# Kernel tuning notes

Measured on AMD Instinct MI355X. Metric: run time of the kernel, lower is better.

## Reference

```python
import jax, jax.numpy as jnp
import numpy as np

N_LAYERS = 5
D = 300        # pretrained GIN hidden dim
D_HID = 600
BN_EPS = 1e-5
IN_DIM = 256
HID = 128
OUT_DIM = 1


def setup_inputs() -> dict:
    key = jax.random.key(0)
    ks = jax.random.split(key, 24)
    N, E, G = 200_000, 800_000, 8192
    s = 0.02
    return {
        # graph structure / categorical features
        "atomic_number": jax.random.randint(ks[0], (N,), 0, 120),
        "chirality_type": jax.random.randint(ks[1], (N,), 0, 3),
        "bond_type": jax.random.randint(ks[2], (E,), 0, 6),
        "bond_direction_type": jax.random.randint(ks[3], (E,), 0, 3),
        "src": jax.random.randint(ks[4], (E,), 0, N),
        "dst": jax.random.randint(ks[5], (E,), 0, N),
        "graph_id": jnp.sort(jax.random.randint(ks[6], (N,), 0, G)),
        "n_graphs": G,
        # pretrained GIN params
        "emb_atom": jax.random.normal(ks[7], (120, D)) * s,
        "emb_chir": jax.random.normal(ks[8], (3, D)) * s,
        "edge_bond": jax.random.normal(ks[9], (N_LAYERS, 6, D)) * s,
        "edge_dir": jax.random.normal(ks[10], (N_LAYERS, 3, D)) * s,
        "W1": jax.random.normal(ks[11], (N_LAYERS, D, D_HID)) * s,
        "b1": jnp.zeros((N_LAYERS, D_HID)),
        "W2": jax.random.normal(ks[12], (N_LAYERS, D_HID, D)) * s,
        "b2": jnp.zeros((N_LAYERS, D)),
        "bn_gamma": jnp.ones((N_LAYERS, D)),
        "bn_beta": jnp.zeros((N_LAYERS, D)),
        "bn_mean": jax.random.normal(ks[13], (N_LAYERS, D)) * s,
        "bn_var": jax.random.uniform(ks[14], (N_LAYERS, D), minval=0.5, maxval=1.5),
        # head params
        "Wt": jax.random.normal(ks[15], (D, IN_DIM)) * s,
        "bt": jnp.zeros((IN_DIM,)),
        "Wh": jax.random.normal(ks[16], (IN_DIM, HID)) * s,
        "bh": jnp.zeros((HID,)),
        "Wf": jax.random.normal(ks[17], (HID, OUT_DIM)) * s,
        "bf": jnp.zeros((OUT_DIM,)),
    }


def reference(atomic_number, chirality_type, bond_type, bond_direction_type,
              src, dst, graph_id, n_graphs,
              emb_atom, emb_chir, edge_bond, edge_dir,
              W1, b1, W2, b2, bn_gamma, bn_beta, bn_mean, bn_var,
              Wt, bt, Wh, bh, Wf, bf):
    N = atomic_number.shape[0]
    # input node embedding (sum of categorical embeddings)
    h = emb_atom[atomic_number] + emb_chir[chirality_type]  # [N, D]

    for l in range(N_LAYERS):
        e = edge_bond[l][bond_type] + edge_dir[l][bond_direction_type]  # [E, D]
        msg = h[src] + e                                                # gather
        agg = jax.ops.segment_sum(msg, dst, num_segments=N)             # scatter-add
        z = h + agg                                                     # GIN eps=0 self term
        z = jax.nn.relu(z @ W1[l] + b1[l]) @ W2[l] + b2[l]              # MLP 300->600->300
        # BatchNorm in eval mode (running stats)
        z = (z - bn_mean[l]) * (bn_gamma[l] / jnp.sqrt(bn_var[l] + BN_EPS)) + bn_beta[l]
        h = jax.nn.relu(z) if l < N_LAYERS - 1 else z

    # AvgPooling readout: segment mean per graph
    sums = jax.ops.segment_sum(h, graph_id, num_segments=n_graphs)      # [G, D]
    cnts = jax.ops.segment_sum(jnp.ones((N,), h.dtype), graph_id, num_segments=n_graphs)
    x = sums / jnp.maximum(cnts, 1.0)[:, None]

    x = x @ Wt + bt                      # transform: Linear(300, in_dim)
    x = jax.nn.leaky_relu(x @ Wh + bh)   # hidden layer + LeakyReLU
    # dropout is identity in eval mode
    return x @ Wf + bf                   # [G, out_dim]
```

## Files before the change

### kernel.cpp

```cpp
#include <hip/hip_runtime.h>
#include <hip/hip_bf16.h>

#define D_NODE 300
#define DHID   600
#define NLAYER 5
#define NG     8192
#define BN_EPS 1e-5f
#define KP1    320
#define KP2    608
#define PER1   (DHID * KP1)
#define PER2   (D_NODE * KP2)

typedef unsigned short u16;
typedef unsigned int   u32;
typedef unsigned long long u64;
using f32x4   = __attribute__((ext_vector_type(4))) float;
using short8  = __attribute__((ext_vector_type(8))) short;
using short4v = __attribute__((ext_vector_type(4))) short;

__device__ __forceinline__ float bf2f(u16 u) {
    union { unsigned int i; float f; } v; v.i = ((unsigned int)u) << 16; return v.f;
}
__device__ __forceinline__ u16 f2bf(float f) {
    union { float f; unsigned int i; } v; v.f = f;
    unsigned int x = v.i;
    return (u16)((x + 0x7FFFu + ((x >> 16) & 1u)) >> 16);
}

__global__ __launch_bounds__(256) void embed_kernel(
    const int* __restrict__ an, const int* __restrict__ ct,
    const float* __restrict__ emb_atom, const float* __restrict__ emb_chir,
    u16* __restrict__ h, long total)
{
    long idx = (long)blockIdx.x * blockDim.x + threadIdx.x;
    if (idx >= total) return;
    int n = (int)(idx / 75);
    int c = (int)(idx % 75);
    int a = an[n], cc = ct[n];
    const float4 av = *(const float4*)&emb_atom[(long)a * D_NODE + c * 4];
    const float4 cv = *(const float4*)&emb_chir[(long)cc * D_NODE + c * 4];
    ushort4 o;
    o.x = f2bf(av.x + cv.x);
    o.y = f2bf(av.y + cv.y);
    o.z = f2bf(av.z + cv.z);
    o.w = f2bf(av.w + cv.w);
    *(ushort4*)&h[(long)n * D_NODE + c * 4] = o;
}

__global__ __launch_bounds__(256) void wconv_split(
    const float* __restrict__ W, u16* __restrict__ WbT,
    int K, int N, int KP, long per, long total)
{
    long idx = (long)blockIdx.x * blockDim.x + threadIdx.x;
    if (idx >= total) return;
    int l = (int)(idx / per);
    long r = idx % per;
    int n = (int)(r / KP);
    int k = (int)(r % KP);
    float v = (k < K) ? W[(long)l * K * N + (long)k * N + n] : 0.f;
    u16 hi = f2bf(v);
    float lo = v - bf2f(hi);
    WbT[(long)(2 * l) * per + r]     = hi;
    WbT[(long)(2 * l + 1) * per + r] = f2bf(lo);
}

__global__ __launch_bounds__(256) void comb_kernel(
    const float* __restrict__ ebond, const float* __restrict__ edir,
    float* __restrict__ comb, long total)
{
    long idx = (long)blockIdx.x * blockDim.x + threadIdx.x;
    if (idx >= total) return;
    int l  = (int)(idx / (18 * 75));
    int r  = (int)(idx % (18 * 75));
    int cm = r / 75;
    int c4 = r % 75;
    const float4 eb = *(const float4*)&ebond[((long)l * 6 + cm / 3) * D_NODE + c4 * 4];
    const float4 ed = *(const float4*)&edir [((long)l * 3 + cm % 3) * D_NODE + c4 * 4];
    float4 o;
    o.x = eb.x + ed.x; o.y = eb.y + ed.y; o.z = eb.z + ed.z; o.w = eb.w + ed.w;
    *(float4*)&comb[((long)l * 18 + cm) * D_NODE + c4 * 4] = o;
}

__global__ __launch_bounds__(256) void zero_int_kernel(int* __restrict__ p, int n)
{
    int i = blockIdx.x * blockDim.x + threadIdx.x;
    if (i < n) p[i] = 0;
}
__global__ __launch_bounds__(256) void count_kernel(
    const int* __restrict__ dst, int* __restrict__ cnt, int E)
{
    int e = blockIdx.x * blockDim.x + threadIdx.x;
    if (e < E) atomicAdd(&cnt[dst[e]], 1);
}
__global__ __launch_bounds__(256) void scan1_kernel(
    const int* __restrict__ cnt, int* __restrict__ bsum, int N)
{
    __shared__ int red[256];
    int b = blockIdx.x, t = threadIdx.x;
    int i0 = b * 1024 + t * 4;
    int s = 0;
    #pragma unroll
    for (int j = 0; j < 4; ++j) { int i = i0 + j; if (i < N) s += cnt[i]; }
    red[t] = s; __syncthreads();
    for (int off = 128; off > 0; off >>= 1) {
        if (t < off) red[t] += red[t + off];
        __syncthreads();
    }
    if (t == 0) bsum[b] = red[0];
}
__global__ void scan2_kernel(int* __restrict__ bsum, int nb)
{
    if (threadIdx.x == 0 && blockIdx.x == 0) {
        int run = 0;
        for (int b = 0; b < nb; ++b) { int v = bsum[b]; bsum[b] = run; run += v; }
    }
}
__global__ __launch_bounds__(256) void scan3_kernel(
    const int* __restrict__ bsum, int* __restrict__ cnt,
    int* __restrict__ row_ptr, int N, int E)
{
    __shared__ int sbuf[256];
    int b = blockIdx.x, t = threadIdx.x;
    int i0 = b * 1024 + t * 4;
    int v[4]; int s = 0;
    #pragma unroll
    for (int j = 0; j < 4; ++j) { int i = i0 + j; v[j] = (i < N) ? cnt[i] : 0; s += v[j]; }
    sbuf[t] = s; __syncthreads();
    for (int off = 1; off < 256; off <<= 1) {
        int add = (t >= off) ? sbuf[t - off] : 0;
        __syncthreads();
        sbuf[t] += add;
        __syncthreads();
    }
    int base = bsum[b] + sbuf[t] - s;
    #pragma unroll
    for (int j = 0; j < 4; ++j) {
        int i = i0 + j;
        if (i < N) { row_ptr[i] = base; cnt[i] = base; base += v[j]; }
    }
    if (b == 0 && t == 0) row_ptr[N] = E;
}
__global__ __launch_bounds__(256) void fill_kernel(
    const int* __restrict__ src, const int* __restrict__ bt, const int* __restrict__ bd,
    const int* __restrict__ dst, int* __restrict__ fillp,
    u32* __restrict__ epack, int E)
{
    int e = blockIdx.x * blockDim.x + threadIdx.x;
    if (e < E) {
        int pos = atomicAdd(&fillp[dst[e]], 1);
        epack[pos] = (u32)src[e] | ((u32)(bt[e] * 3 + bd[e]) << 20);
    }
}

__global__ __launch_bounds__(256) void agg_kernel(
    const u16* __restrict__ h,
    const int* __restrict__ row_ptr, const u32* __restrict__ epack,
    const float* __restrict__ comb,
    u16* __restrict__ z, long total)
{
    long idx = (long)blockIdx.x * blockDim.x + threadIdx.x;
    if (idx >= total) return;
    int n = (int)(idx / 75);
    int c = (int)(idx % 75);
    const ushort4 hq = *(const ushort4*)&h[(long)n * D_NODE + c * 4];
    float a0 = bf2f(hq.x), a1 = bf2f(hq.y), a2 = bf2f(hq.z), a3 = bf2f(hq.w);
    int s0 = row_ptr[n], s1 = row_ptr[n + 1];
    for (int i = s0; i < s1; ++i) {
        u32 ep = epack[i];
        int s  = (int)(ep & 0xFFFFFu);
        int cm = (int)(ep >> 20);
        const ushort4 hv = *(const ushort4*)&h[(long)s * D_NODE + c * 4];
        const float4 cv = *(const float4*)&comb[(long)cm * D_NODE + c * 4];
        a0 += bf2f(hv.x) + cv.x;
        a1 += bf2f(hv.y) + cv.y;
        a2 += bf2f(hv.z) + cv.z;
        a3 += bf2f(hv.w) + cv.w;
    }
    ushort4 o;
    o.x = f2bf(a0); o.y = f2bf(a1); o.z = f2bf(a2); o.w = f2bf(a3);
    *(ushort4*)&z[(long)n * D_NODE + c * 4] = o;
}

__global__ __launch_bounds__(512, 1) void mlp_fused(
    const u16* __restrict__ Z,
    const u16* __restrict__ W1T,
    const u16* __restrict__ W2T,
    const float* __restrict__ b1, const float* __restrict__ b2,
    const float* __restrict__ bn_g, const float* __restrict__ bn_b,
    const float* __restrict__ bn_m, const float* __restrict__ bn_v,
    u16* __restrict__ Hout, int Nrows, int relu_out)
{
    __shared__ u16 As[128][328];
    __shared__ u16 Tc[128][136];
    const int tid  = threadIdx.x;
    const int lane = tid & 63;
    const int w    = tid >> 6;
    const int lrow = lane & 15;
    const int kg   = lane >> 4;
    const long r0  = (long)blockIdx.x * 128;
    const short8 zz = (short8){0,0,0,0,0,0,0,0};

    for (int i = tid; i < 128 * 80; i += 512) {
        int r = i / 80, c4 = i % 80;
        short4v v = (short4v){0, 0, 0, 0};
        if (c4 < 75 && r0 + r < Nrows)
            v = *(const short4v*)&Z[(r0 + r) * D_NODE + c4 * 4];
        *(short4v*)&As[r][c4 * 4] = v;
    }
    __syncthreads();

    f32x4 hacc[8][3];
    #pragma unroll
    for (int m = 0; m < 8; ++m)
        #pragma unroll
        for (int n = 0; n < 3; ++n)
            hacc[m][n] = (f32x4){0.f, 0.f, 0.f, 0.f};
    const u16* w2p[3]; bool w2v[3];
    #pragma unroll
    for (int nf = 0; nf < 3; ++nf) {
        int gn = w * 48 + nf * 16 + lrow;
        w2v[nf] = (gn < D_NODE);
        w2p[nf] = W2T + (long)gn * KP2 + kg * 8;
    }
    const bool p2_active = (w * 48 < D_NODE);

    for (int tc = 0; tc < 5; ++tc) {
        const int gn1 = tc * 128 + w * 16 + lrow;
        const bool v1 = (gn1 < DHID);
        const u16* w1p = W1T + (long)gn1 * KP1 + kg * 8;

        f32x4 p1[8];
        #pragma unroll
        for (int m = 0; m < 8; ++m) p1[m] = (f32x4){0.f, 0.f, 0.f, 0.f};

        short8 cwh = v1 ? *(const short8*)(w1p) : zz;

        #pragma unroll
        for (int k0i = 0; k0i < 10; ++k0i) {
            short8 nwh;
            if (k0i < 9) {
                nwh = v1 ? *(const short8*)(w1p + (k0i + 1) * 32) : zz;
            }
            {
                short8 a0 = *(const short8*)&As[ 0 + lrow][k0i * 32 + kg * 8];
                short8 a1 = *(const short8*)&As[16 + lrow][k0i * 32 + kg * 8];
                short8 a2 = *(const short8*)&As[32 + lrow][k0i * 32 + kg * 8];
                short8 a3 = *(const short8*)&As[48 + lrow][k0i * 32 + kg * 8];
                __builtin_amdgcn_s_setprio(1);
                p1[0] = __builtin_amdgcn_mfma_f32_16x16x32_bf16(a0, cwh, p1[0], 0, 0, 0);
                p1[1] = __builtin_amdgcn_mfma_f32_16x16x32_bf16(a1, cwh, p1[1], 0, 0, 0);
                p1[2] = __builtin_amdgcn_mfma_f32_16x16x32_bf16(a2, cwh, p1[2], 0, 0, 0);
                p1[3] = __builtin_amdgcn_mfma_f32_16x16x32_bf16(a3, cwh, p1[3], 0, 0, 0);
                __builtin_amdgcn_s_setprio(0);
            }
            {
                short8 a4 = *(const short8*)&As[ 64 + lrow][k0i * 32 + kg * 8];
                short8 a5 = *(const short8*)&As[ 80 + lrow][k0i * 32 + kg * 8];
                short8 a6 = *(const short8*)&As[ 96 + lrow][k0i * 32 + kg * 8];
                short8 a7 = *(const short8*)&As[112 + lrow][k0i * 32 + kg * 8];
                __builtin_amdgcn_s_setprio(1);
                p1[4] = __builtin_amdgcn_mfma_f32_16x16x32_bf16(a4, cwh, p1[4], 0, 0, 0);
                p1[5] = __builtin_amdgcn_mfma_f32_16x16x32_bf16(a5, cwh, p1[5], 0, 0, 0);
                p1[6] = __builtin_amdgcn_mfma_f32_16x16x32_bf16(a6, cwh, p1[6], 0, 0, 0);
                p1[7] = __builtin_amdgcn_mfma_f32_16x16x32_bf16(a7, cwh, p1[7], 0, 0, 0);
                __builtin_amdgcn_s_setprio(0);
            }
            if (k0i < 9) { cwh = nwh; }
        }

        {
            float bias = v1 ? b1[gn1] : 0.f;
            #pragma unroll
            for (int m = 0; m < 8; ++m)
                #pragma unroll
                for (int j = 0; j < 4; ++j) {
                    float v = fmaxf(p1[m][j] + bias, 0.f);
                    Tc[m * 16 + kg * 4 + j][w * 16 + lrow] = f2bf(v);
                }
        }
        __syncthreads();

        if (p2_active) {
            const int kbase = tc * 128;
            #pragma unroll
            for (int ks = 0; ks < 4; ++ks) {
                if (kbase + ks * 32 < KP2) {
                    const int kk = kbase + ks * 32;
                    short8 w2h0 = w2v[0] ? *(const short8*)(w2p[0] + kk) : zz;
                    short8 w2h1 = w2v[1] ? *(const short8*)(w2p[1] + kk) : zz;
                    short8 w2h2 = w2v[2] ? *(const short8*)(w2p[2] + kk) : zz;
                    {
                        short8 t0 = *(const short8*)&Tc[ 0 + lrow][ks * 32 + kg * 8];
                        short8 t1 = *(const short8*)&Tc[16 + lrow][ks * 32 + kg * 8];
                        short8 t2 = *(const short8*)&Tc[32 + lrow][ks * 32 + kg * 8];
                        short8 t3 = *(const short8*)&Tc[48 + lrow][ks * 32 + kg * 8];
                        __builtin_amdgcn_s_setprio(1);
                        hacc[0][0] = __builtin_amdgcn_mfma_f32_16x16x32_bf16(t0, w2h0, hacc[0][0], 0, 0, 0);
                        hacc[1][0] = __builtin_amdgcn_mfma_f32_16x16x32_bf16(t1, w2h0, hacc[1][0], 0, 0, 0);
                        hacc[2][0] = __builtin_amdgcn_mfma_f32_16x16x32_bf16(t2, w2h0, hacc[2][0], 0, 0, 0);
                        hacc[3][0] = __builtin_amdgcn_mfma_f32_16x16x32_bf16(t3, w2h0, hacc[3][0], 0, 0, 0);
                        hacc[0][1] = __builtin_amdgcn_mfma_f32_16x16x32_bf16(t0, w2h1, hacc[0][1], 0, 0, 0);
                        hacc[1][1] = __builtin_amdgcn_mfma_f32_16x16x32_bf16(t1, w2h1, hacc[1][1], 0, 0, 0);
                        hacc[2][1] = __builtin_amdgcn_mfma_f32_16x16x32_bf16(t2, w2h1, hacc[2][1], 0, 0, 0);
                        hacc[3][1] = __builtin_amdgcn_mfma_f32_16x16x32_bf16(t3, w2h1, hacc[3][1], 0, 0, 0);
                        hacc[0][2] = __builtin_amdgcn_mfma_f32_16x16x32_bf16(t0, w2h2, hacc[0][2], 0, 0, 0);
                        hacc[1][2] = __builtin_amdgcn_mfma_f32_16x16x32_bf16(t1, w2h2, hacc[1][2], 0, 0, 0);
                        hacc[2][2] = __builtin_amdgcn_mfma_f32_16x16x32_bf16(t2, w2h2, hacc[2][2], 0, 0, 0);
                        hacc[3][2] = __builtin_amdgcn_mfma_f32_16x16x32_bf16(t3, w2h2, hacc[3][2], 0, 0, 0);
                        __builtin_amdgcn_s_setprio(0);
                    }
                    {
                        short8 t4 = *(const short8*)&Tc[ 64 + lrow][ks * 32 + kg * 8];
                        short8 t5 = *(const short8*)&Tc[ 80 + lrow][ks * 32 + kg * 8];
                        short8 t6 = *(const short8*)&Tc[ 96 + lrow][ks * 32 + kg * 8];
                        short8 t7 = *(const short8*)&Tc[112 + lrow][ks * 32 + kg * 8];
                        __builtin_amdgcn_s_setprio(1);
                        hacc[4][0] = __builtin_amdgcn_mfma_f32_16x16x32_bf16(t4, w2h0, hacc[4][0], 0, 0, 0);
                        hacc[5][0] = __builtin_amdgcn_mfma_f32_16x16x32_bf16(t5, w2h0, hacc[5][0], 0, 0, 0);
                        hacc[6][0] = __builtin_amdgcn_mfma_f32_16x16x32_bf16(t6, w2h0, hacc[6][0], 0, 0, 0);
                        hacc[7][0] = __builtin_amdgcn_mfma_f32_16x16x32_bf16(t7, w2h0, hacc[7][0], 0, 0, 0);
                        hacc[4][1] = __builtin_amdgcn_mfma_f32_16x16x32_bf16(t4, w2h1, hacc[4][1], 0, 0, 0);
                        hacc[5][1] = __builtin_amdgcn_mfma_f32_16x16x32_bf16(t5, w2h1, hacc[5][1], 0, 0, 0);
                        hacc[6][1] = __builtin_amdgcn_mfma_f32_16x16x32_bf16(t6, w2h1, hacc[6][1], 0, 0, 0);
                        hacc[7][1] = __builtin_amdgcn_mfma_f32_16x16x32_bf16(t7, w2h1, hacc[7][1], 0, 0, 0);
                        hacc[4][2] = __builtin_amdgcn_mfma_f32_16x16x32_bf16(t4, w2h2, hacc[4][2], 0, 0, 0);
                        hacc[5][2] = __builtin_amdgcn_mfma_f32_16x16x32_bf16(t5, w2h2, hacc[5][2], 0, 0, 0);
                        hacc[6][2] = __builtin_amdgcn_mfma_f32_16x16x32_bf16(t6, w2h2, hacc[6][2], 0, 0, 0);
                        hacc[7][2] = __builtin_amdgcn_mfma_f32_16x16x32_bf16(t7, w2h2, hacc[7][2], 0, 0, 0);
                        __builtin_amdgcn_s_setprio(0);
                    }
                }
            }
        }
        __syncthreads();
    }

    #pragma unroll
    for (int nf = 0; nf < 3; ++nf) {
        int gn = w * 48 + nf * 16 + lrow;
        if (gn < D_NODE) {
            float bias = b2[gn];
            float sc = bn_g[gn] * rsqrtf(bn_v[gn] + BN_EPS);
            float mn = bn_m[gn], bb = bn_b[gn];
            #pragma unroll
            for (int m = 0; m < 8; ++m)
                #pragma unroll
                for (int j = 0; j < 4; ++j) {
                    long gr = r0 + m * 16 + kg * 4 + j;
                    if (gr < Nrows) {
                        float v = hacc[m][nf][j] + bias;
                        v = (v - mn) * sc + bb;
                        if (relu_out) v = fmaxf(v, 0.f);
                        Hout[gr * D_NODE + gn] = f2bf(v);
                    }
                }
        }
    }
}

__device__ __forceinline__ int lower_bound(const int* __restrict__ a, int n, int key)
{
    int lo = 0, hi = n;
    while (lo < hi) { int mid = (lo + hi) >> 1; if (a[mid] < key) lo = mid + 1; else hi = mid; }
    return lo;
}

__global__ __launch_bounds__(256) void pool_head1(
    const u16* __restrict__ h, const int* __restrict__ gid, int N,
    const float* __restrict__ Wt, const float* __restrict__ bt,
    float* __restrict__ x1)
{
    __shared__ float xs[304];
    __shared__ int se[2];
    int g = blockIdx.x;
    int t = threadIdx.x;
    if (t == 0) se[0] = lower_bound(gid, N, g);
    if (t == 1) se[1] = lower_bound(gid, N, g + 1);
    __syncthreads();
    int start = se[0], end = se[1];
    float inv = (end > start) ? 1.0f / (float)(end - start) : 0.f;
    float a0 = 0.f, a1 = 0.f;
    for (int n = start; n < end; ++n) {
        const u16* hp = &h[(long)n * D_NODE];
        a0 += bf2f(hp[t]);
        if (t < 44) a1 += bf2f(hp[256 + t]);
    }
    xs[t] = a0 * inv;
    if (t < 44) xs[256 + t] = a1 * inv;
    __syncthreads();
    float acc = bt[t];
    for (int k = 0; k < D_NODE; ++k)
        acc = fmaf(xs[k], Wt[(long)k * 256 + t], acc);
    x1[(long)g * 256 + t] = acc;
}

__global__ __launch_bounds__(128) void head2_kernel(
    const float* __restrict__ x1,
    const float* __restrict__ Wh, const float* __restrict__ bh,
    const float* __restrict__ Wf, const float* __restrict__ bf,
    float* __restrict__ out, int G)
{
    __shared__ float xs[256];
    __shared__ float red[128];
    int g = blockIdx.x;
    int t = threadIdx.x;
    for (int i = t; i < 256; i += 128) xs[i] = x1[(long)g * 256 + i];
    __syncthreads();
    float acc = bh[t];
    for (int k = 0; k < 256; ++k)
        acc = fmaf(xs[k], Wh[(long)k * 128 + t], acc);
    acc = acc > 0.f ? acc : 0.01f * acc;
    red[t] = acc * Wf[t];
    __syncthreads();
    for (int s = 64; s > 0; s >>= 1) {
        if (t < s) red[t] += red[t + s];
        __syncthreads();
    }
    if (t == 0) out[g] = red[0] + bf[0];
}

extern "C" void kernel_launch(void* const* d_in, const int* in_sizes, int n_in,
                              void* d_out, int out_size, void* d_ws, size_t ws_size,
                              hipStream_t stream)
{
    const int* an   = (const int*)d_in[0];
    const int* ct   = (const int*)d_in[1];
    const int* bt   = (const int*)d_in[2];
    const int* bd   = (const int*)d_in[3];
    const int* src  = (const int*)d_in[4];
    const int* dst  = (const int*)d_in[5];
    const int* gid  = (const int*)d_in[6];
    const float* emb_atom  = (const float*)d_in[8];
    const float* emb_chir  = (const float*)d_in[9];
    const float* edge_bond = (const float*)d_in[10];
    const float* edge_dir  = (const float*)d_in[11];
    const float* W1   = (const float*)d_in[12];
    const float* b1   = (const float*)d_in[13];
    const float* W2   = (const float*)d_in[14];
    const float* b2   = (const float*)d_in[15];
    const float* bn_g = (const float*)d_in[16];
    const float* bn_b = (const float*)d_in[17];
    const float* bn_m = (const float*)d_in[18];
    const float* bn_v = (const float*)d_in[19];
    const float* Wt   = (const float*)d_in[20];
    const float* btr  = (const float*)d_in[21];
    const float* Wh   = (const float*)d_in[22];
    const float* bh   = (const float*)d_in[23];
    const float* Wf   = (const float*)d_in[24];
    const float* bf   = (const float*)d_in[25];

    const long N = in_sizes[0];
    const long E = in_sizes[4];
    const int  G = NG;

    char* base = (char*)d_ws;
    size_t off = 0;
    u16* h  = (u16*)(base + off);           off += (size_t)N * D_NODE * 2;
    u16* z  = (u16*)(base + off);           off += (size_t)N * D_NODE * 2;
    u16* WbT1 = (u16*)(base + off);         off += (size_t)NLAYER * 2 * PER1 * 2;
    u16* WbT2 = (u16*)(base + off);         off += (size_t)NLAYER * 2 * PER2 * 2;
    float* comb = (float*)(base + off);     off += (size_t)NLAYER * 18 * D_NODE * 4;
    int* row_ptr = (int*)(base + off);      off += (((size_t)(N + 1) * 4) + 63) & ~(size_t)63;
    u32* epack = (u32*)(base + off);
    int* row_fill = (int*)z;
    int* bsum     = row_fill + N;
    float* x1     = (float*)z;

    const long nodeTot = N * 75;
    const int  blk = 256;
    const long nodeBlocks = (nodeTot + blk - 1) / blk;
    const int  SB = (int)((N + 1023) / 1024);

    {
        long t1 = (long)NLAYER * PER1;
        wconv_split<<<(t1 + blk - 1) / blk, blk, 0, stream>>>(
            W1, WbT1, D_NODE, DHID, KP1, (long)PER1, t1);
        long t2 = (long)NLAYER * PER2;
        wconv_split<<<(t2 + blk - 1) / blk, blk, 0, stream>>>(
            W2, WbT2, DHID, D_NODE, KP2, (long)PER2, t2);
    }
    {
        long tc = (long)NLAYER * 18 * 75;
        comb_kernel<<<(tc + blk - 1) / blk, blk, 0, stream>>>(
            edge_bond, edge_dir, comb, tc);
    }

    zero_int_kernel<<<((int)N + blk - 1) / blk, blk, 0, stream>>>(row_fill, (int)N);
    count_kernel<<<((int)E + blk - 1) / blk, blk, 0, stream>>>(dst, row_fill, (int)E);
    scan1_kernel<<<SB, blk, 0, stream>>>(row_fill, bsum, (int)N);
    scan2_kernel<<<1, 64, 0, stream>>>(bsum, SB);
    scan3_kernel<<<SB, blk, 0, stream>>>(bsum, row_fill, row_ptr, (int)N, (int)E);
    fill_kernel<<<((int)E + blk - 1) / blk, blk, 0, stream>>>(
        src, bt, bd, dst, row_fill, epack, (int)E);

    embed_kernel<<<nodeBlocks, blk, 0, stream>>>(an, ct, emb_atom, emb_chir, h, nodeTot);

    const int mlpBlocks = (int)((N + 127) / 128);
    for (int l = 0; l < NLAYER; ++l) {
        agg_kernel<<<nodeBlocks, blk, 0, stream>>>(
            h, row_ptr, epack,
            comb + (long)l * 18 * D_NODE,
            z, nodeTot);

        mlp_fused<<<mlpBlocks, 512, 0, stream>>>(
            z,
            WbT1 + (long)(2 * l) * PER1,
            WbT2 + (long)(2 * l) * PER2,
            b1 + (long)l * DHID, b2 + (long)l * D_NODE,
            bn_g + (long)l * D_NODE, bn_b + (long)l * D_NODE,
            bn_m + (long)l * D_NODE, bn_v + (long)l * D_NODE,
            h, (int)N, (l < NLAYER - 1) ? 1 : 0);
    }

    pool_head1<<<G, 256, 0, stream>>>(h, gid, (int)N, Wt, btr, x1);
    head2_kernel<<<G, 128, 0, stream>>>(x1, Wh, bh, Wf, bf, (float*)d_out, G);
}
```

Before: 2.919 ms.

## Warp-specialize fused MLP into producer/consumer waves with double-buffered hidden tile

The fused MLP kernel grows from 512 to 1024 threads. Eight waves now compute the first GEMM plus ReLU into a double-buffered shared-memory hidden tile, while eight other waves run the second GEMM on the previous tile, so the two GEMMs overlap instead of alternating. The BN/ReLU epilogue is staged through the reused input tile so global stores are coalesced row-wise. The costs are a higher register budget per thread at 1024 threads, which risks spills given the 96-float accumulators, and a larger LDS footprint.

```diff
diff --git a/kernel.cpp b/kernel.cpp
--- a/kernel.cpp
+++ b/kernel.cpp
@@ -181,7 +181,7 @@
     *(ushort4*)&z[(long)n * D_NODE + c * 4] = o;
 }
 
-__global__ __launch_bounds__(512, 1) void mlp_fused(
+__global__ __launch_bounds__(1024, 1) void mlp_fused(
     const u16* __restrict__ Z,
     const u16* __restrict__ W1T,
     const u16* __restrict__ W2T,
@@ -191,16 +191,16 @@
     u16* __restrict__ Hout, int Nrows, int relu_out)
 {
     __shared__ u16 As[128][328];
-    __shared__ u16 Tc[128][136];
+    __shared__ u16 Tc[2][128][136];
     const int tid  = threadIdx.x;
     const int lane = tid & 63;
-    const int w    = tid >> 6;
+    const int wid  = tid >> 6;
     const int lrow = lane & 15;
     const int kg   = lane >> 4;
     const long r0  = (long)blockIdx.x * 128;
     const short8 zz = (short8){0,0,0,0,0,0,0,0};
 
-    for (int i = tid; i < 128 * 80; i += 512) {
+    for (int i = tid; i < 128 * 80; i += 1024) {
         int r = i / 80, c4 = i % 80;
         short4v v = (short4v){0, 0, 0, 0};
         if (c4 < 75 && r0 + r < Nrows)
@@ -209,152 +209,154 @@
     }
     __syncthreads();
 
-    f32x4 hacc[8][3];
-    #pragma unroll
-    for (int m = 0; m < 8; ++m)
-        #pragma unroll
-        for (int n = 0; n < 3; ++n)
-            hacc[m][n] = (f32x4){0.f, 0.f, 0.f, 0.f};
-    const u16* w2p[3]; bool w2v[3];
-    #pragma unroll
-    for (int nf = 0; nf < 3; ++nf) {
-        int gn = w * 48 + nf * 16 + lrow;
-        w2v[nf] = (gn < D_NODE);
-        w2p[nf] = W2T + (long)gn * KP2 + kg * 8;
-    }
-    const bool p2_active = (w * 48 < D_NODE);
-
-    for (int tc = 0; tc < 5; ++tc) {
-        const int gn1 = tc * 128 + w * 16 + lrow;
-        const bool v1 = (gn1 < DHID);
-        const u16* w1p = W1T + (long)gn1 * KP1 + kg * 8;
-
-        f32x4 p1[8];
-        #pragma unroll
-        for (int m = 0; m < 8; ++m) p1[m] = (f32x4){0.f, 0.f, 0.f, 0.f};
-
-        short8 cwh = v1 ? *(const short8*)(w1p) : zz;
-
-        #pragma unroll
-        for (int k0i = 0; k0i < 10; ++k0i) {
-            short8 nwh;
-            if (k0i < 9) {
-                nwh = v1 ? *(const short8*)(w1p + (k0i + 1) * 32) : zz;
+    if (wid < 8) {
+        #pragma unroll 1
+        for (int tc = 0; tc < 5; ++tc) {
+            const int gn1 = tc * 128 + wid * 16 + lrow;
+            const bool v1 = (gn1 < DHID);
+            const u16* w1p = W1T + (long)gn1 * KP1 + kg * 8;
+
+            f32x4 p1[8];
+            #pragma unroll
+            for (int m = 0; m < 8; ++m) p1[m] = (f32x4){0.f, 0.f, 0.f, 0.f};
+
+            short8 cwh = v1 ? *(const short8*)(w1p) : zz;
+
+            #pragma unroll
+            for (int k0i = 0; k0i < 10; ++k0i) {
+                short8 nwh;
+                if (k0i < 9) {
+                    nwh = v1 ? *(const short8*)(w1p + (k0i + 1) * 32) : zz;
+                }
+                short8 a[8];
+                #pragma unroll
+                for (int m = 0; m < 8; ++m)
+                    a[m] = *(const short8*)&As[m * 16 + lrow][k0i * 32 + kg * 8];
+
+                __builtin_amdgcn_s_setprio(1);
+                #pragma unroll
+                for (int m = 0; m < 8; ++m)
+                    p1[m] = __builtin_amdgcn_mfma_f32_16x16x32_bf16(a[m], cwh, p1[m], 0, 0, 0);
+                __builtin_amdgcn_s_setprio(0);
+
+                if (k0i < 9) { cwh = nwh; }
             }
+
             {
-                short8 a0 = *(const short8*)&As[ 0 + lrow][k0i * 32 + kg * 8];
-                short8 a1 = *(const short8*)&As[16 + lrow][k0i * 32 + kg * 8];
-                short8 a2 = *(const short8*)&As[32 + lrow][k0i * 32 + kg * 8];
-                short8 a3 = *(const short8*)&As[48 + lrow][k0i * 32 + kg * 8];
-                __builtin_amdgcn_s_setprio(1);
-                p1[0] = __builtin_amdgcn_mfma_f32_16x16x32_bf16(a0, cwh, p1[0], 0, 0, 0);
-                p1[1] = __builtin_amdgcn_mfma_f32_16x16x32_bf16(a1, cwh, p1[1], 0, 0, 0);
-                p1[2] = __builtin_amdgcn_mfma_f32_16x16x32_bf16(a2, cwh, p1[2], 0, 0, 0);
-                p1[3] = __builtin_amdgcn_mfma_f32_16x16x32_bf16(a3, cwh, p1[3], 0, 0, 0);
-                __builtin_amdgcn_s_setprio(0);
+                float bias = v1 ? b1[gn1] : 0.f;
+                #pragma unroll
+                for (int m = 0; m < 8; ++m)
+                    #pragma unroll
+                    for (int j = 0; j < 4; ++j) {
+                        float v = fmaxf(p1[m][j] + bias, 0.f);
+                        Tc[tc & 1][m * 16 + kg * 4 + j][wid * 16 + lrow] = f2bf(v);
+                    }
             }
-            {
-                short8 a4 = *(const short8*)&As[ 64 + lrow][k0i * 32 + kg * 8];
-                short8 a5 = *(const short8*)&As[ 80 + lrow][k0i * 32 + kg * 8];
-                short8 a6 = *(const short8*)&As[ 96 + lrow][k0i * 32 + kg * 8];
-                short8 a7 = *(const short8*)&As[112 + lrow][k0i * 32 + kg * 8];
-                __builtin_amdgcn_s_setprio(1);
-                p1[4] = __builtin_amdgcn_mfma_f32_16x16x32_bf16(a4, cwh, p1[4], 0, 0, 0);
-                p1[5] = __builtin_amdgcn_mfma_f32_16x16x32_bf16(a5, cwh, p1[5], 0, 0, 0);
-                p1[6] = __builtin_amdgcn_mfma_f32_16x16x32_bf16(a6, cwh, p1[6], 0, 0, 0);
-                p1[7] = __builtin_amdgcn_mfma_f32_16x16x32_bf16(a7, cwh, p1[7], 0, 0, 0);
-                __builtin_amdgcn_s_setprio(0);
-            }
-            if (k0i < 9) { cwh = nwh; }
-        }
-
-        {
-            float bias = v1 ? b1[gn1] : 0.f;
-            #pragma unroll
-            for (int m = 0; m < 8; ++m)
-                #pragma unroll
-                for (int j = 0; j < 4; ++j) {
-                    float v = fmaxf(p1[m][j] + bias, 0.f);
-                    Tc[m * 16 + kg * 4 + j][w * 16 + lrow] = f2bf(v);
-                }
+            __syncthreads();
         }
         __syncthreads();
-
-        if (p2_active) {
-            const int kbase = tc * 128;
+    } else {
+        const int cw = wid - 8;
+        f32x4 hacc[8][3];
+        #pragma unroll
+        for (int m = 0; m < 8; ++m)
             #pragma unroll
-            for (int ks = 0; ks < 4; ++ks) {
-                if (kbase + ks * 32 < KP2) {
-                    const int kk = kbase + ks * 32;
-                    short8 w2h0 = w2v[0] ? *(const short8*)(w2p[0] + kk) : zz;
-                    short8 w2h1 = w2v[1] ? *(const short8*)(w2p[1] + kk) : zz;
-                    short8 w2h2 = w2v[2] ? *(const short8*)(w2p[2] + kk) : zz;
-                    {
-                        short8 t0 = *(const short8*)&Tc[ 0 + lrow][ks * 32 + kg * 8];
-                        short8 t1 = *(const short8*)&Tc[16 + lrow][ks * 32 + kg * 8];
-                        short8 t2 = *(const short8*)&Tc[32 + lrow][ks * 32 + kg * 8];
-                        short8 t3 = *(const short8*)&Tc[48 + lrow][ks * 32 + kg * 8];
-                        __builtin_amdgcn_s_setprio(1);
-                        hacc[0][0] = __builtin_amdgcn_mfma_f32_16x16x32_bf16(t0, w2h0, hacc[0][0], 0, 0, 0);
-                        hacc[1][0] = __builtin_amdgcn_mfma_f32_16x16x32_bf16(t1, w2h0, hacc[1][0], 0, 0, 0);
-                        hacc[2][0] = __builtin_amdgcn_mfma_f32_16x16x32_bf16(t2, w2h0, hacc[2][0], 0, 0, 0);
-                        hacc[3][0] = __builtin_amdgcn_mfma_f32_16x16x32_bf16(t3, w2h0, hacc[3][0], 0, 0, 0);
-                        hacc[0][1] = __builtin_amdgcn_mfma_f32_16x16x32_bf16(t0, w2h1, hacc[0][1], 0, 0, 0);
-                        hacc[1][1] = __builtin_amdgcn_mfma_f32_16x16x32_bf16(t1, w2h1, hacc[1][1], 0, 0, 0);
-                        hacc[2][1] = __builtin_amdgcn_mfma_f32_16x16x32_bf16(t2, w2h1, hacc[2][1], 0, 0, 0);
-                        hacc[3][1] = __builtin_amdgcn_mfma_f32_16x16x32_bf16(t3, w2h1, hacc[3][1], 0, 0, 0);
-                        hacc[0][2] = __builtin_amdgcn_mfma_f32_16x16x32_bf16(t0, w2h2, hacc[0][2], 0, 0, 0);
-                        hacc[1][2] = __builtin_amdgcn_mfma_f32_16x16x32_bf16(t1, w2h2, hacc[1][2], 0, 0, 0);
-                        hacc[2][2] = __builtin_amdgcn_mfma_f32_16x16x32_bf16(t2, w2h2, hacc[2][2], 0, 0, 0);
-                        hacc[3][2] = __builtin_amdgcn_mfma_f32_16x16x32_bf16(t3, w2h2, hacc[3][2], 0, 0, 0);
-                        __builtin_amdgcn_s_setprio(0);
-                    }
-                    {
-                        short8 t4 = *(const short8*)&Tc[ 64 + lrow][ks * 32 + kg * 8];
-                        short8 t5 = *(const short8*)&Tc[ 80 + lrow][ks * 32 + kg * 8];
-                        short8 t6 = *(const short8*)&Tc[ 96 + lrow][ks * 32 + kg * 8];
-                        short8 t7 = *(const short8*)&Tc[112 + lrow][ks * 32 + kg * 8];
-                        __builtin_amdgcn_s_setprio(1);
-                        hacc[4][0] = __builtin_amdgcn_mfma_f32_16x16x32_bf16(t4, w2h0, hacc[4][0], 0, 0, 0);
-                        hacc[5][0] = __builtin_amdgcn_mfma_f32_16x16x32_bf16(t5, w2h0, hacc[5][0], 0, 0, 0);
-                        hacc[6][0] = __builtin_amdgcn_mfma_f32_16x16x32_bf16(t6, w2h0, hacc[6][0], 0, 0, 0);
-                        hacc[7][0] = __builtin_amdgcn_mfma_f32_16x16x32_bf16(t7, w2h0, hacc[7][0], 0, 0, 0);
-                        hacc[4][1] = __builtin_amdgcn_mfma_f32_16x16x32_bf16(t4, w2h1, hacc[4][1], 0, 0, 0);
-                        hacc[5][1] = __builtin_amdgcn_mfma_f32_16x16x32_bf16(t5, w2h1, hacc[5][1], 0, 0, 0);
-                        hacc[6][1] = __builtin_amdgcn_mfma_f32_16x16x32_bf16(t6, w2h1, hacc[6][1], 0, 0, 0);
-                        hacc[7][1] = __builtin_amdgcn_mfma_f32_16x16x32_bf16(t7, w2h1, hacc[7][1], 0, 0, 0);
-                        hacc[4][2] = __builtin_amdgcn_mfma_f32_16x16x32_bf16(t4, w2h2, hacc[4][2], 0, 0, 0);
-                        hacc[5][2] = __builtin_amdgcn_mfma_f32_16x16x32_bf16(t5, w2h2, hacc[5][2], 0, 0, 0);
-                        hacc[6][2] = __builtin_amdgcn_mfma_f32_16x16x32_bf16(t6, w2h2, hacc[6][2], 0, 0, 0);
-                        hacc[7][2] = __builtin_amdgcn_mfma_f32_16x16x32_bf16(t7, w2h2, hacc[7][2], 0, 0, 0);
-                        __builtin_amdgcn_s_setprio(0);
+            for (int n = 0; n < 3; ++n)
+                hacc[m][n] = (f32x4){0.f, 0.f, 0.f, 0.f};
+        const u16* w2p[3]; bool w2v[3];
+        #pragma unroll
+        for (int nf = 0; nf < 3; ++nf) {
+            int gn = cw * 48 + nf * 16 + lrow;
+            w2v[nf] = (gn < D_NODE);
+            w2p[nf] = W2T + (long)gn * KP2 + kg * 8;
+        }
+        const bool p2_active = (cw * 48 < D_NODE);
+
+        __syncthreads();
+        #pragma unroll 1
+        for (int tc = 0; tc < 5; ++tc) {
+            if (p2_active) {
+                const int kbase = tc * 128;
+                const int rb = tc & 1;
+                #pragma unroll
+                for (int ks = 0; ks < 4; ++ks) {
+                    if (kbase + ks * 32 < KP2) {
+                        const int kk = kbase + ks * 32;
+                        short8 w2h0 = w2v[0] ? *(const short8*)(w2p[0] + kk) : zz;
+                        short8 w2h1 = w2v[1] ? *(const short8*)(w2p[1] + kk) : zz;
+                        short8 w2h2 = w2v[2] ? *(const short8*)(w2p[2] + kk) : zz;
+                        {
+                            short8 t0 = *(const short8*)&Tc[rb][ 0 + lrow][ks * 32 + kg * 8];
+                            short8 t1 = *(const short8*)&Tc[rb][16 + lrow][ks * 32 + kg * 8];
+                            short8 t2 = *(const short8*)&Tc[rb][32 + lrow][ks * 32 + kg * 8];
+                            short8 t3 = *(const short8*)&Tc[rb][48 + lrow][ks * 32 + kg * 8];
+                            __builtin_amdgcn_s_setprio(1);
+                            hacc[0][0] = __builtin_amdgcn_mfma_f32_16x16x32_bf16(t0, w2h0, hacc[0][0], 0, 0, 0);
+                            hacc[1][0] = __builtin_amdgcn_mfma_f32_16x16x32_bf16(t1, w2h0, hacc[1][0], 0, 0, 0);
+                            hacc[2][0] = __builtin_amdgcn_mfma_f32_16x16x32_bf16(t2, w2h0, hacc[2][0], 0, 0, 0);
+                            hacc[3][0] = __builtin_amdgcn_mfma_f32_16x16x32_bf16(t3, w2h0, hacc[3][0], 0, 0, 0);
+                            hacc[0][1] = __builtin_amdgcn_mfma_f32_16x16x32_bf16(t0, w2h1, hacc[0][1], 0, 0, 0);
+                            hacc[1][1] = __builtin_amdgcn_mfma_f32_16x16x32_bf16(t1, w2h1, hacc[1][1], 0, 0, 0);
+                            hacc[2][1] = __builtin_amdgcn_mfma_f32_16x16x32_bf16(t2, w2h1, hacc[2][1], 0, 0, 0);
+                            hacc[3][1] = __builtin_amdgcn_mfma_f32_16x16x32_bf16(t3, w2h1, hacc[3][1], 0, 0, 0);
+                            hacc[0][2] = __builtin_amdgcn_mfma_f32_16x16x32_bf16(t0, w2h2, hacc[0][2], 0, 0, 0);
+                            hacc[1][2] = __builtin_amdgcn_mfma_f32_16x16x32_bf16(t1, w2h2, hacc[1][2], 0, 0, 0);
+                            hacc[2][2] = __builtin_amdgcn_mfma_f32_16x16x32_bf16(t2, w2h2, hacc[2][2], 0, 0, 0);
+                            hacc[3][2] = __builtin_amdgcn_mfma_f32_16x16x32_bf16(t3, w2h2, hacc[3][2], 0, 0, 0);
+                            __builtin_amdgcn_s_setprio(0);
+                        }
+                        {
+                            short8 t4 = *(const short8*)&Tc[rb][ 64 + lrow][ks * 32 + kg * 8];
+                            short8 t5 = *(const short8*)&Tc[rb][ 80 + lrow][ks * 32 + kg * 8];
+                            short8 t6 = *(const short8*)&Tc[rb][ 96 + lrow][ks * 32 + kg * 8];
+                            short8 t7 = *(const short8*)&Tc[rb][112 + lrow][ks * 32 + kg * 8];
+                            __builtin_amdgcn_s_setprio(1);
+                            hacc[4][0] = __builtin_amdgcn_mfma_f32_16x16x32_bf16(t4, w2h0, hacc[4][0], 0, 0, 0);
+                            hacc[5][0] = __builtin_amdgcn_mfma_f32_16x16x32_bf16(t5, w2h0, hacc[5][0], 0, 0, 0);
+                            hacc[6][0] = __builtin_amdgcn_mfma_f32_16x16x32_bf16(t6, w2h0, hacc[6][0], 0, 0, 0);
+                            hacc[7][0] = __builtin_amdgcn_mfma_f32_16x16x32_bf16(t7, w2h0, hacc[7][0], 0, 0, 0);
+                            hacc[4][1] = __builtin_amdgcn_mfma_f32_16x16x32_bf16(t4, w2h1, hacc[4][1], 0, 0, 0);
+                            hacc[5][1] = __builtin_amdgcn_mfma_f32_16x16x32_bf16(t5, w2h1, hacc[5][1], 0, 0, 0);
+                            hacc[6][1] = __builtin_amdgcn_mfma_f32_16x16x32_bf16(t6, w2h1, hacc[6][1], 0, 0, 0);
+                            hacc[7][1] = __builtin_amdgcn_mfma_f32_16x16x32_bf16(t7, w2h1, hacc[7][1], 0, 0, 0);
+                            hacc[4][2] = __builtin_amdgcn_mfma_f32_16x16x32_bf16(t4, w2h2, hacc[4][2], 0, 0, 0);
+                            hacc[5][2] = __builtin_amdgcn_mfma_f32_16x16x32_bf16(t5, w2h2, hacc[5][2], 0, 0, 0);
+                            hacc[6][2] = __builtin_amdgcn_mfma_f32_16x16x32_bf16(t6, w2h2, hacc[6][2], 0, 0, 0);
+                            hacc[7][2] = __builtin_amdgcn_mfma_f32_16x16x32_bf16(t7, w2h2, hacc[7][2], 0, 0, 0);
+                            __builtin_amdgcn_s_setprio(0);
+                        }
                     }
                 }
             }
-        }
-        __syncthreads();
-    }
-
-    #pragma unroll
-    for (int nf = 0; nf < 3; ++nf) {
-        int gn = w * 48 + nf * 16 + lrow;
-        if (gn < D_NODE) {
-            float bias = b2[gn];
-            float sc = bn_g[gn] * rsqrtf(bn_v[gn] + BN_EPS);
-            float mn = bn_m[gn], bb = bn_b[gn];
-            #pragma unroll
-            for (int m = 0; m < 8; ++m)
+            if (tc == 4 && p2_active) {
                 #pragma unroll
-                for (int j = 0; j < 4; ++j) {
-                    long gr = r0 + m * 16 + kg * 4 + j;
-                    if (gr < Nrows) {
-                        float v = hacc[m][nf][j] + bias;
-                        v = (v - mn) * sc + bb;
-                        if (relu_out) v = fmaxf(v, 0.f);
-                        Hout[gr * D_NODE + gn] = f2bf(v);
+                for (int nf = 0; nf < 3; ++nf) {
+                    int gn = cw * 48 + nf * 16 + lrow;
+                    if (gn < D_NODE) {
+                        float bias = b2[gn];
+                        float sc = bn_g[gn] * rsqrtf(bn_v[gn] + BN_EPS);
+                        float mn = bn_m[gn], bb = bn_b[gn];
+                        #pragma unroll
+                        for (int m = 0; m < 8; ++m)
+                            #pragma unroll
+                            for (int j = 0; j < 4; ++j) {
+                                float v = hacc[m][nf][j] + bias;
+                                v = (v - mn) * sc + bb;
+                                if (relu_out) v = fmaxf(v, 0.f);
+                                As[m * 16 + kg * 4 + j][gn] = f2bf(v);
+                            }
                     }
                 }
+            }
+            __syncthreads();
         }
+    }
+
+    for (int i = tid; i < 128 * 75; i += 1024) {
+        int r = i / 75, c4 = i % 75;
+        long gr = r0 + r;
+        if (gr < Nrows)
+            *(ushort4*)&Hout[gr * D_NODE + c4 * 4] = *(const ushort4*)&As[r][c4 * 4];
     }
 }
 
@@ -502,7 +504,7 @@
             comb + (long)l * 18 * D_NODE,
             z, nodeTot);
 
-        mlp_fused<<<mlpBlocks, 512, 0, stream>>>(
+        mlp_fused<<<mlpBlocks, 1024, 0, stream>>>(
             z,
             WbT1 + (long)(2 * l) * PER1,
             WbT2 + (long)(2 * l) * PER2,
```

Measured after the change: 3.718 ms. +27.4%, slower.
